# Performance work log

Hardware: AMD Instinct MI355X
Metric: run time of the kernel (lower is better)

## Reference

```python
import jax, jax.numpy as jnp
import numpy as np

B, S, D = 64, 2048, 512


def setup_inputs() -> dict:
    key = jax.random.key(0)
    ks = jax.random.split(key, 7)
    return {
        "c_i_1": jax.random.normal(ks[0], (B, D), dtype=jnp.float32),
        "q": jax.random.normal(ks[1], (B, D), dtype=jnp.float32),
        "cw_s": jax.random.normal(ks[2], (B, S, D), dtype=jnp.float32),
        "W_d2d": jax.random.normal(ks[3], (D, 2 * D), dtype=jnp.float32) * 0.02,
        "b_d": jax.random.normal(ks[4], (D,), dtype=jnp.float32) * 0.02,
        "W_1d": jax.random.normal(ks[5], (1, D), dtype=jnp.float32) * 0.02,
        "b_1": jax.random.normal(ks[6], (1,), dtype=jnp.float32) * 0.02,
    }


def reference(c_i_1, q, cw_s, W_d2d, b_d, W_1d, b_1):
    # concat previous control with question rep: [B, 2D]
    conc_cq = jnp.concatenate([c_i_1, q], axis=1)
    # small GEMM + bias: [B, D]
    cq_i = conc_cq @ W_d2d.T + b_d
    # broadcast multiply against contextual word states: [B, S, D]
    cqcw = cw_s * cq_i[:, None, :]
    # projection to attention logits: [B, S, 1]
    ca_is = jnp.einsum("bsd,od->bso", cqcw, W_1d) + b_1
    # attention over the sequence axis
    cv_is = jax.nn.softmax(ca_is, axis=1)
    # weighted sum -> new control state [B, D]
    c_i = jnp.sum(cv_is * cw_s, axis=1)
    return c_i
```

## Files before the change

### kernel.cpp

```cpp
#include <hip/hip_runtime.h>
#include <math.h>

#define BB 64
#define SS 2048
#define DD 512
#define CH 32
#define ROWS (SS/CH)
#define WROWS (ROWS/4)
#define RPI 2
#define ITERS (WROWS/RPI)

__global__ __launch_bounds__(128) void k_w(
    const float* __restrict__ c1, const float* __restrict__ q,
    const float* __restrict__ Wd, const float* __restrict__ bd,
    const float* __restrict__ W1, float* __restrict__ w)
{
    __shared__ float conc[2*DD];
    const int b = blockIdx.y;
    const int t = threadIdx.x;
    for (int i = t; i < DD; i += 128) {
        conc[i]      = c1[b*DD + i];
        conc[DD + i] = q[b*DD + i];
    }
    __syncthreads();
    const int d = blockIdx.x * 128 + t;
    const float4* Wr = (const float4*)(Wd + (size_t)d * (2*DD));
    const float4* cc = (const float4*)conc;
    float acc = 0.f;
    #pragma unroll 8
    for (int k = 0; k < (2*DD)/4; ++k) {
        float4 a = Wr[k];
        float4 c = cc[k];
        acc += a.x*c.x + a.y*c.y + a.z*c.z + a.w*c.w;
    }
    w[b*DD + d] = (acc + bd[d]) * W1[d];
}

__global__ __launch_bounds__(256, 6) void k_pass(
    const float* __restrict__ cw, const float* __restrict__ w,
    float* __restrict__ pm, float* __restrict__ pl, float* __restrict__ pacc)
{
    const int blk  = blockIdx.x;
    const int b    = blk >> 5;
    const int ch   = blk & (CH - 1);
    const int tid  = threadIdx.x;
    const int wave = tid >> 6;
    const int lane = tid & 63;

    const float4* wb = (const float4*)(w + b*DD);
    const float4 w0 = wb[lane];
    const float4 w1 = wb[64 + lane];

    const float* rb = cw + ((size_t)b*SS + (size_t)ch*ROWS + (size_t)wave*WROWS) * DD;

    float m = -INFINITY, l = 0.f;
    float4 a0 = make_float4(0,0,0,0), a1 = make_float4(0,0,0,0);

    #pragma unroll
    for (int i = 0; i < ITERS; ++i) {
        float4 c0[RPI], c1v[RPI];
        #pragma unroll
        for (int r = 0; r < RPI; ++r) {
            const float4* p = (const float4*)(rb + (size_t)(i*RPI + r) * DD);
            c0[r]  = p[lane];
            c1v[r] = p[64 + lane];
        }

        float d_[RPI];
        #pragma unroll
        for (int r = 0; r < RPI; ++r) {
            d_[r] = c0[r].x*w0.x + c0[r].y*w0.y + c0[r].z*w0.z + c0[r].w*w0.w
                  + c1v[r].x*w1.x + c1v[r].y*w1.y + c1v[r].z*w1.z + c1v[r].w*w1.w;
        }
        #pragma unroll
        for (int off = 32; off; off >>= 1) {
            #pragma unroll
            for (int r = 0; r < RPI; ++r) d_[r] += __shfl_xor(d_[r], off, 64);
        }

        const float mn = fmaxf(fmaxf(d_[0], d_[1]), m);
        const float alpha = __expf(m - mn);
        m = mn;
        const float p0 = __expf(d_[0] - m);
        const float p1 = __expf(d_[1] - m);
        l = l*alpha + p0 + p1;
        a0.x = a0.x*alpha + p0*c0[0].x  + p1*c0[1].x;
        a0.y = a0.y*alpha + p0*c0[0].y  + p1*c0[1].y;
        a0.z = a0.z*alpha + p0*c0[0].z  + p1*c0[1].z;
        a0.w = a0.w*alpha + p0*c0[0].w  + p1*c0[1].w;
        a1.x = a1.x*alpha + p0*c1v[0].x + p1*c1v[1].x;
        a1.y = a1.y*alpha + p0*c1v[0].y + p1*c1v[1].y;
        a1.z = a1.z*alpha + p0*c1v[0].z + p1*c1v[1].z;
        a1.w = a1.w*alpha + p0*c1v[0].w + p1*c1v[1].w;
    }

    __shared__ float lm[4], ll[4];
    __shared__ float lacc[4][DD];
    if (lane == 0) lm[wave] = m;
    __syncthreads();
    const float M = fmaxf(fmaxf(lm[0], lm[1]), fmaxf(lm[2], lm[3]));
    const float beta = __expf(m - M);
    float4* lw = (float4*)lacc[wave];
    lw[lane]      = make_float4(a0.x*beta, a0.y*beta, a0.z*beta, a0.w*beta);
    lw[64 + lane] = make_float4(a1.x*beta, a1.y*beta, a1.z*beta, a1.w*beta);
    if (lane == 0) ll[wave] = l * beta;
    __syncthreads();
    const float s0 = lacc[0][tid]     + lacc[1][tid]     + lacc[2][tid]     + lacc[3][tid];
    const float s1 = lacc[0][tid+256] + lacc[1][tid+256] + lacc[2][tid+256] + lacc[3][tid+256];
    pacc[(size_t)blk*DD + tid]       = s0;
    pacc[(size_t)blk*DD + tid + 256] = s1;
    if (tid == 0) {
        pm[blk] = M;
        pl[blk] = ll[0] + ll[1] + ll[2] + ll[3];
    }
}

__global__ __launch_bounds__(256) void k_comb(
    const float* __restrict__ pm, const float* __restrict__ pl,
    const float* __restrict__ pacc, float* __restrict__ out)
{
    const int b = blockIdx.x;
    const int tid = threadIdx.x;
    float M = -INFINITY;
    #pragma unroll
    for (int p = 0; p < CH; ++p) M = fmaxf(M, pm[b*CH + p]);
    float L = 0.f;
    float sx = 0.f, sy = 0.f;
    #pragma unroll
    for (int p = 0; p < CH; ++p) {
        const float sc = __expf(pm[b*CH + p] - M);
        L += pl[b*CH + p] * sc;
        const float2 v = ((const float2*)(pacc + (size_t)(b*CH + p)*DD))[tid];
        sx += sc * v.x;
        sy += sc * v.y;
    }
    const float inv = 1.f / L;
    ((float2*)(out + b*DD))[tid] = make_float2(sx*inv, sy*inv);
}

extern "C" void kernel_launch(void* const* d_in, const int* in_sizes, int n_in,
                              void* d_out, int out_size, void* d_ws, size_t ws_size,
                              hipStream_t stream)
{
    const float* c1 = (const float*)d_in[0];
    const float* q  = (const float*)d_in[1];
    const float* cw = (const float*)d_in[2];
    const float* Wd = (const float*)d_in[3];
    const float* bd = (const float*)d_in[4];
    const float* W1 = (const float*)d_in[5];

    float* out  = (float*)d_out;
    float* ws   = (float*)d_ws;
    float* w    = ws;
    float* pm   = w  + BB*DD;
    float* pl   = pm + BB*CH;
    float* pacc = pl + BB*CH;

    k_w   <<<dim3(DD/128, BB), 128, 0, stream>>>(c1, q, Wd, bd, W1, w);
    k_pass<<<BB*CH,            256, 0, stream>>>(cw, w, pm, pl, pacc);
    k_comb<<<BB,               256, 0, stream>>>(pm, pl, pacc, out);
}
```

Before: 455.7 us.

## Double-buffer row loads in k_pass with register ping-pong and sched barriers

Halves the number of sequence chunks per batch, processes four rows per step instead of two, and adds a software-pipelined ping-pong of register buffers. The next group of rows is loaded before the current group is computed, with sched_barrier hints keeping the loads issued early. Occupancy is lowered to 4 blocks per CU to make room for the extra registers. The aim is to hide global memory latency on this bandwidth-bound streaming pass, at the cost of fewer resident waves and fewer total blocks.

After: 486.9 us. 1.07x slower.

```diff
diff --git a/kernel.cpp b/kernel.cpp
--- a/kernel.cpp
+++ b/kernel.cpp
@@ -4,10 +4,10 @@
 #define BB 64
 #define SS 2048
 #define DD 512
-#define CH 32
+#define CH 16
 #define ROWS (SS/CH)
 #define WROWS (ROWS/4)
-#define RPI 2
+#define RPI 4
 #define ITERS (WROWS/RPI)
 
 __global__ __launch_bounds__(128) void k_w(
@@ -36,12 +36,51 @@
     w[b*DD + d] = (acc + bd[d]) * W1[d];
 }
 
-__global__ __launch_bounds__(256, 6) void k_pass(
+
+#define LOADG(DST0, DST1, g)                                                  \
+    {   const float* nb_ = rb + (size_t)(g) * RPI * DD;                       \
+        _Pragma("unroll")                                                     \
+        for (int r = 0; r < RPI; ++r) {                                       \
+            const float4* p_ = (const float4*)(nb_ + (size_t)r * DD);         \
+            DST0[r] = p_[lane];                                               \
+            DST1[r] = p_[64 + lane];                                          \
+        } }
+
+#define STEP(C0, C1)                                                          \
+    {   float d_[RPI];                                                        \
+        _Pragma("unroll")                                                     \
+        for (int r = 0; r < RPI; ++r)                                         \
+            d_[r] = C0[r].x*w0.x + C0[r].y*w0.y + C0[r].z*w0.z + C0[r].w*w0.w \
+                  + C1[r].x*w1.x + C1[r].y*w1.y + C1[r].z*w1.z + C1[r].w*w1.w;\
+        _Pragma("unroll")                                                     \
+        for (int off = 32; off; off >>= 1) {                                  \
+            _Pragma("unroll")                                                 \
+            for (int r = 0; r < RPI; ++r) d_[r] += __shfl_xor(d_[r], off, 64);\
+        }                                                                     \
+        float mn = fmaxf(fmaxf(d_[0], d_[1]), fmaxf(d_[2], d_[3]));           \
+        mn = fmaxf(mn, m);                                                    \
+        const float alpha = __expf(m - mn);                                   \
+        m = mn;                                                               \
+        float pr[RPI];                                                        \
+        _Pragma("unroll")                                                     \
+        for (int r = 0; r < RPI; ++r) pr[r] = __expf(d_[r] - m);              \
+        l = l*alpha + (pr[0] + pr[1] + pr[2] + pr[3]);                        \
+        a0.x *= alpha; a0.y *= alpha; a0.z *= alpha; a0.w *= alpha;           \
+        a1.x *= alpha; a1.y *= alpha; a1.z *= alpha; a1.w *= alpha;           \
+        _Pragma("unroll")                                                     \
+        for (int r = 0; r < RPI; ++r) {                                       \
+            a0.x += pr[r]*C0[r].x; a0.y += pr[r]*C0[r].y;                     \
+            a0.z += pr[r]*C0[r].z; a0.w += pr[r]*C0[r].w;                     \
+            a1.x += pr[r]*C1[r].x; a1.y += pr[r]*C1[r].y;                     \
+            a1.z += pr[r]*C1[r].z; a1.w += pr[r]*C1[r].w;                     \
+        } }
+
+__global__ __launch_bounds__(256, 4) void k_pass(
     const float* __restrict__ cw, const float* __restrict__ w,
     float* __restrict__ pm, float* __restrict__ pl, float* __restrict__ pacc)
 {
     const int blk  = blockIdx.x;
-    const int b    = blk >> 5;
+    const int b    = blk >> 4;
     const int ch   = blk & (CH - 1);
     const int tid  = threadIdx.x;
     const int wave = tid >> 6;
@@ -53,45 +92,22 @@
 
     const float* rb = cw + ((size_t)b*SS + (size_t)ch*ROWS + (size_t)wave*WROWS) * DD;
 
+    float4 A0[RPI], A1[RPI], B0[RPI], B1[RPI];
+    LOADG(A0, A1, 0);
+
     float m = -INFINITY, l = 0.f;
     float4 a0 = make_float4(0,0,0,0), a1 = make_float4(0,0,0,0);
 
     #pragma unroll
-    for (int i = 0; i < ITERS; ++i) {
-        float4 c0[RPI], c1v[RPI];
-        #pragma unroll
-        for (int r = 0; r < RPI; ++r) {
-            const float4* p = (const float4*)(rb + (size_t)(i*RPI + r) * DD);
-            c0[r]  = p[lane];
-            c1v[r] = p[64 + lane];
+    for (int i = 0; i < ITERS; i += 2) {
+        LOADG(B0, B1, i + 1);
+        __builtin_amdgcn_sched_barrier(0);
+        STEP(A0, A1);
+        if (i + 2 < ITERS) {
+            LOADG(A0, A1, i + 2);
         }
-
-        float d_[RPI];
-        #pragma unroll
-        for (int r = 0; r < RPI; ++r) {
-            d_[r] = c0[r].x*w0.x + c0[r].y*w0.y + c0[r].z*w0.z + c0[r].w*w0.w
-                  + c1v[r].x*w1.x + c1v[r].y*w1.y + c1v[r].z*w1.z + c1v[r].w*w1.w;
-        }
-        #pragma unroll
-        for (int off = 32; off; off >>= 1) {
-            #pragma unroll
-            for (int r = 0; r < RPI; ++r) d_[r] += __shfl_xor(d_[r], off, 64);
-        }
-
-        const float mn = fmaxf(fmaxf(d_[0], d_[1]), m);
-        const float alpha = __expf(m - mn);
-        m = mn;
-        const float p0 = __expf(d_[0] - m);
-        const float p1 = __expf(d_[1] - m);
-        l = l*alpha + p0 + p1;
-        a0.x = a0.x*alpha + p0*c0[0].x  + p1*c0[1].x;
-        a0.y = a0.y*alpha + p0*c0[0].y  + p1*c0[1].y;
-        a0.z = a0.z*alpha + p0*c0[0].z  + p1*c0[1].z;
-        a0.w = a0.w*alpha + p0*c0[0].w  + p1*c0[1].w;
-        a1.x = a1.x*alpha + p0*c1v[0].x + p1*c1v[1].x;
-        a1.y = a1.y*alpha + p0*c1v[0].y + p1*c1v[1].y;
-        a1.z = a1.z*alpha + p0*c1v[0].z + p1*c1v[1].z;
-        a1.w = a1.w*alpha + p0*c1v[0].w + p1*c1v[1].w;
+        __builtin_amdgcn_sched_barrier(0);
+        STEP(B0, B1);
     }
 
     __shared__ float lm[4], ll[4];
```
